# Optimization experiments

Measured on AMD Instinct MI355X. Metric: run time of the kernel, lower is better.

## Reference

```python
import jax, jax.numpy as jnp
import numpy as np

# Config mirrors CrossAttentionAudio2T(dim=768, n_head=12, num_frames=16, spec_frames=8,
# attn_all_frame=True, audio_patch=196, time_encoding=False, use_stpos=True)
B, T, N, NA, ST, D, H = 4, 8, 196, 196, 8, 768, 12
HD = D // H
SCALE = HD ** -0.5


def setup_inputs() -> dict:
    key = jax.random.key(0)
    ks = jax.random.split(key, 12)
    r = lambda k, s: jax.random.normal(k, s, dtype=jnp.float32)
    return dict(
        t_x=r(ks[0], (B, T * N, D)),
        audio=r(ks[1], (NA + 2, B * ST, D)),
        vmae_space_pos=SCALE * r(ks[2], (N, D)),
        audio_space_pos=SCALE * r(ks[3], (NA, D)),
        vmae_temporal_pos=SCALE * r(ks[4], (T, D)),
        audio_temporal_pos=SCALE * r(ks[5], (ST, D)),
        q_w=0.02 * r(ks[6], (D, D)),
        q_b=jnp.zeros((D,), jnp.float32),
        kv_w=0.02 * r(ks[7], (2 * D, D)),
        kv_b=jnp.zeros((2 * D,), jnp.float32),
        proj_w=0.02 * r(ks[8], (D, D)),
        proj_b=jnp.zeros((D,), jnp.float32),
    )


def reference(t_x, audio, vmae_space_pos, audio_space_pos, vmae_temporal_pos,
              audio_temporal_pos, q_w, q_b, kv_w, kv_b, proj_w, proj_b):
    # --- video query tokens: add spatial + temporal pos embeds ---
    x = t_x.reshape(B, T, N, D) + vmae_space_pos          # [B,T,N,D] + [N,D]
    x = x.transpose(0, 2, 1, 3) + vmae_temporal_pos       # [B,N,T,D] + [T,D]
    x = x.transpose(0, 2, 1, 3).reshape(B, T * N, D)      # 'b n t d -> b (t n) d'

    # --- audio key/value tokens: drop 2 lead tokens, add pos embeds ---
    a = audio[2:].reshape(NA, B, ST, D).transpose(1, 2, 0, 3)  # 'n (b t) d -> b t n d'
    a = a + audio_space_pos                                    # [B,ST,NA,D] + [NA,D]
    a = a.transpose(0, 2, 1, 3) + audio_temporal_pos           # [B,NA,ST,D] + [ST,D]
    a = a.reshape(B, NA * ST, D)                               # 'b n t d -> b (n t) d'

    # --- projections ---
    q = (x @ q_w.T + q_b).reshape(B, T * N, H, HD).transpose(0, 2, 1, 3)   # [B,H,Lq,HD]
    kv = (a @ kv_w.T + kv_b).reshape(B, NA * ST, 2, H, HD)
    k = kv[:, :, 0].transpose(0, 2, 1, 3)                                  # [B,H,Lk,HD]
    v = kv[:, :, 1].transpose(0, 2, 1, 3)

    # --- scaled dot-product cross-attention (full score matrix, as in source) ---
    attn = jax.nn.softmax(jnp.einsum('bhqd,bhkd->bhqk', q * SCALE, k), axis=-1)
    o = jnp.einsum('bhqk,bhkd->bhqd', attn, v)
    o = o.transpose(0, 2, 1, 3).reshape(B, T * N, D)
    return o @ proj_w.T + proj_b
```

## Files before the change

### kernel.cpp

```cpp
#include <hip/hip_runtime.h>

typedef short s8v __attribute__((ext_vector_type(8)));
typedef short s4v __attribute__((ext_vector_type(4)));
typedef float f4v __attribute__((ext_vector_type(4)));

#define LQ 1568
#define LK 1568
#define NH 12

__device__ __forceinline__ unsigned short f2bf(float f) {
  union { float f; unsigned u; } x; x.f = f;
  unsigned r = x.u + 0x7FFFu + ((x.u >> 16) & 1u);
  return (unsigned short)(r >> 16);
}


__global__ void prep_x(const float* __restrict__ t_x, const float* __restrict__ sp,
                       const float* __restrict__ tp, unsigned short* __restrict__ xb,
                       int total4) {
  int i = blockIdx.x * 256 + threadIdx.x;
  if (i >= total4) return;
  int d4 = (i % 192) * 4;
  int row = i / 192;
  int l = row % LQ;
  int t = l / 196, n = l % 196;
  float4 a  = *(const float4*)(t_x + (size_t)i * 4);
  float4 s  = *(const float4*)(sp + n * 768 + d4);
  float4 tt = *(const float4*)(tp + t * 768 + d4);
  ushort4 o;
  o.x = f2bf(a.x + s.x + tt.x);
  o.y = f2bf(a.y + s.y + tt.y);
  o.z = f2bf(a.z + s.z + tt.z);
  o.w = f2bf(a.w + s.w + tt.w);
  *(ushort4*)(xb + (size_t)i * 4) = o;
}

__global__ void prep_a(const float* __restrict__ audio, const float* __restrict__ asp,
                       const float* __restrict__ atp, unsigned short* __restrict__ ab,
                       int total4) {
  int i = blockIdx.x * 256 + threadIdx.x;
  if (i >= total4) return;
  int d4 = (i % 192) * 4;
  int row = i / 192;
  int b = row / LK;
  int r2 = row % LK;
  int na = r2 >> 3, ta = r2 & 7;
  const float* src = audio + ((size_t)(2 + na) * 32 + b * 8 + ta) * 768 + d4;
  float4 a  = *(const float4*)src;
  float4 s  = *(const float4*)(asp + na * 768 + d4);
  float4 tt = *(const float4*)(atp + ta * 768 + d4);
  ushort4 o;
  o.x = f2bf(a.x + s.x + tt.x);
  o.y = f2bf(a.y + s.y + tt.y);
  o.z = f2bf(a.z + s.z + tt.z);
  o.w = f2bf(a.w + s.w + tt.w);
  *(ushort4*)(ab + (size_t)i * 4) = o;
}

__global__ void conv_bf16(const float* __restrict__ src, unsigned short* __restrict__ dst,
                          int n4) {
  int i = blockIdx.x * 256 + threadIdx.x;
  if (i >= n4) return;
  float4 v = *(const float4*)(src + (size_t)i * 4);
  ushort4 o;
  o.x = f2bf(v.x); o.y = f2bf(v.y); o.z = f2bf(v.z); o.w = f2bf(v.w);
  *(ushort4*)(dst + (size_t)i * 4) = o;
}

__global__ __launch_bounds__(256, 2) void gemm_bt(
    const unsigned short* __restrict__ A, const unsigned short* __restrict__ W,
    const float* __restrict__ bias,
    unsigned short* __restrict__ out_a, unsigned short* __restrict__ out_b,
    float* __restrict__ out_f, int K, int N, int mode) {
  __shared__ __align__(16) unsigned short As[128 * 72];
  __shared__ __align__(16) unsigned short Bs[128 * 72];
  const int tid = threadIdx.x;
  const int lane = tid & 63, wave = tid >> 6;
  const int wm = wave & 1, wn = wave >> 1;
  const int l15 = lane & 15, quad = lane >> 4;
  const int row0 = blockIdx.x * 128;
  const int col0 = blockIdx.y * 128;

  f4v acc[4][4] = {};

  for (int k0 = 0; k0 < K; k0 += 64) {
    __syncthreads();
    for (int c = tid; c < 1024; c += 256) {
      int r = c >> 3, kc = c & 7;
      *(uint4*)(As + r * 72 + kc * 8) =
          *(const uint4*)(A + (size_t)(row0 + r) * K + k0 + kc * 8);
      *(uint4*)(Bs + r * 72 + kc * 8) =
          *(const uint4*)(W + (size_t)(col0 + r) * K + k0 + kc * 8);
    }
    __syncthreads();
#pragma unroll
    for (int kk = 0; kk < 2; ++kk) {
      s8v af[4], bf[4];
#pragma unroll
      for (int i = 0; i < 4; ++i) {
        af[i] = *(const s8v*)(As + (wm * 64 + i * 16 + l15) * 72 + kk * 32 + quad * 8);
        bf[i] = *(const s8v*)(Bs + (wn * 64 + i * 16 + l15) * 72 + kk * 32 + quad * 8);
      }
#pragma unroll
      for (int mi = 0; mi < 4; ++mi)
#pragma unroll
        for (int ni = 0; ni < 4; ++ni)
          acc[mi][ni] = __builtin_amdgcn_mfma_f32_16x16x32_bf16(af[mi], bf[ni],
                                                               acc[mi][ni], 0, 0, 0);
    }
  }

#pragma unroll
  for (int mi = 0; mi < 4; ++mi) {
    int rowg = row0 + wm * 64 + mi * 16 + quad * 4;
#pragma unroll
    for (int ni = 0; ni < 4; ++ni) {
      int colg = col0 + wn * 64 + ni * 16 + l15;
      float bv = bias[colg];
      if (mode == 1 && colg >= 768) {
        int oo = colg - 768;
        int h = oo >> 6, hd = oo & 63;
        int b = rowg / LK, l0 = rowg - b * LK;
        ushort4 pk;
        pk.x = f2bf(acc[mi][ni][0] + bv);
        pk.y = f2bf(acc[mi][ni][1] + bv);
        pk.z = f2bf(acc[mi][ni][2] + bv);
        pk.w = f2bf(acc[mi][ni][3] + bv);
        *(ushort4*)(out_b + ((((size_t)b * NH + h) * 392 + (l0 >> 2)) * 64 + hd) * 4) = pk;
        continue;
      }
#pragma unroll
      for (int r = 0; r < 4; ++r) {
        float v = acc[mi][ni][r] + bv;
        int row = rowg + r;
        if (mode == 0) {
          v *= 0.18033688011112042f;
          int b = row / LQ, l = row - b * LQ;
          int h = colg >> 6, hd = colg & 63;
          out_a[(((size_t)b * NH + h) * LQ + l) * 64 + hd] = f2bf(v);
        } else if (mode == 1) {
          int b = row / LK, l = row - b * LK;
          int h = colg >> 6, hd = colg & 63;
          out_a[(((size_t)b * NH + h) * LK + l) * 64 + hd] = f2bf(v);
        } else {
          out_f[(size_t)row * N + colg] = v;
        }
      }
    }
  }
}

__global__ __launch_bounds__(256, 3) void attn(
    const unsigned short* __restrict__ Q, const unsigned short* __restrict__ Kg,
    const unsigned short* __restrict__ Vsw, unsigned short* __restrict__ O) {
  __shared__ __align__(16) unsigned short Kl[112 * 72];
  __shared__ __align__(16) unsigned short Vl[112 * 64];
  const int tid = threadIdx.x;
  const int lane = tid & 63, wave = tid >> 6;
  const int l15 = lane & 15, quad = lane >> 4;
  const int bh = blockIdx.y;
  const int q0 = blockIdx.x * 128;
  const size_t base = (size_t)bh * LK * 64;

  s8v qf[2][2];
#pragma unroll
  for (int mt = 0; mt < 2; ++mt)
#pragma unroll
    for (int kk = 0; kk < 2; ++kk) {
      int row = q0 + wave * 32 + mt * 16 + l15;
      if (row > LQ - 1) row = LQ - 1;
      qf[mt][kk] = *(const s8v*)(Q + base + (size_t)row * 64 + kk * 32 + quad * 8);
    }

  f4v of[2][4] = {};
  float lr[2] = {0.0f, 0.0f};

  for (int k0 = 0; k0 < LK; k0 += 112) {
    __syncthreads();
    for (int c = tid; c < 896; c += 256) {
      int r = c >> 3, kc = c & 7;
      *(uint4*)(Kl + r * 72 + kc * 8) =
          *(const uint4*)(Kg + base + (size_t)(k0 + r) * 64 + kc * 8);
    }
    {
      const uint4* src = (const uint4*)(Vsw + base + (size_t)k0 * 64);
      uint4* dst = (uint4*)Vl;
      for (int c = tid; c < 896; c += 256) dst[c] = src[c];
    }
    __syncthreads();

#pragma unroll
    for (int nt = 0; nt < 7; ++nt) {
      s8v kf0 = *(const s8v*)(Kl + (nt * 16 + l15) * 72 + quad * 8);
      s8v kf1 = *(const s8v*)(Kl + (nt * 16 + l15) * 72 + 32 + quad * 8);
      s4v pf[2];
#pragma unroll
      for (int mt = 0; mt < 2; ++mt) {
        f4v s = {};
        s = __builtin_amdgcn_mfma_f32_16x16x32_bf16(kf0, qf[mt][0], s, 0, 0, 0);
        s = __builtin_amdgcn_mfma_f32_16x16x32_bf16(kf1, qf[mt][1], s, 0, 0, 0);
        float p0 = __builtin_amdgcn_exp2f(s[0]);
        float p1 = __builtin_amdgcn_exp2f(s[1]);
        float p2 = __builtin_amdgcn_exp2f(s[2]);
        float p3 = __builtin_amdgcn_exp2f(s[3]);
        lr[mt] += (p0 + p1) + (p2 + p3);
        union { float f; unsigned u; } a0, a1, a2, a3;
        a0.f = p0; a1.f = p1; a2.f = p2; a3.f = p3;
        union { uint2 u; s4v s; } pk;
        pk.u.x = __builtin_amdgcn_perm(a1.u, a0.u, 0x07060302u);
        pk.u.y = __builtin_amdgcn_perm(a3.u, a2.u, 0x07060302u);
        pf[mt] = pk.s;
      }
#pragma unroll
      for (int nd = 0; nd < 4; ++nd) {
        s4v vf = *(const s4v*)(Vl + ((nt * 4 + quad) << 8) + ((nd * 16 + l15) << 2));
        of[0][nd] = __builtin_amdgcn_mfma_f32_16x16x16bf16_1k(pf[0], vf, of[0][nd], 0, 0, 0);
        of[1][nd] = __builtin_amdgcn_mfma_f32_16x16x16bf16_1k(pf[1], vf, of[1][nd], 0, 0, 0);
      }
    }
  }

#pragma unroll
  for (int mt = 0; mt < 2; ++mt) {
    lr[mt] += __shfl_xor(lr[mt], 16);
    lr[mt] += __shfl_xor(lr[mt], 32);
  }

  const int b = bh / NH, h = bh - b * NH;
#pragma unroll
  for (int mt = 0; mt < 2; ++mt)
#pragma unroll
    for (int r = 0; r < 4; ++r) {
      int row = q0 + wave * 32 + mt * 16 + quad * 4 + r;
      if (row >= LQ) continue;
      float inv = 1.0f / __shfl(lr[mt], quad * 4 + r);
#pragma unroll
      for (int nd = 0; nd < 4; ++nd) {
        float v = of[mt][nd][r] * inv;
        O[((size_t)(b * LQ) + row) * 768 + h * 64 + nd * 16 + l15] = f2bf(v);
      }
    }
}

extern "C" void kernel_launch(void* const* d_in, const int* in_sizes, int n_in,
                              void* d_out, int out_size, void* d_ws, size_t ws_size,
                              hipStream_t stream) {
  const float* t_x    = (const float*)d_in[0];
  const float* audio  = (const float*)d_in[1];
  const float* sp     = (const float*)d_in[2];
  const float* asp    = (const float*)d_in[3];
  const float* tp     = (const float*)d_in[4];
  const float* atp    = (const float*)d_in[5];
  const float* q_w    = (const float*)d_in[6];
  const float* q_b    = (const float*)d_in[7];
  const float* kv_w   = (const float*)d_in[8];
  const float* kv_b   = (const float*)d_in[9];
  const float* proj_w = (const float*)d_in[10];
  const float* proj_b = (const float*)d_in[11];
  float* out = (float*)d_out;

  char* ws = (char*)d_ws;
  size_t off = 0;
  auto alloc = [&](size_t bytes) -> void* {
    void* p = ws + off;
    off += (bytes + 255) & ~(size_t)255;
    return p;
  };
  const size_t TOK = 6272;
  unsigned short* xb  = (unsigned short*)alloc(TOK * 768 * 2);
  unsigned short* ab  = (unsigned short*)alloc(TOK * 768 * 2);
  unsigned short* wq  = (unsigned short*)alloc(768 * 768 * 2);
  unsigned short* wkv = (unsigned short*)alloc(1536 * 768 * 2);
  unsigned short* wp  = (unsigned short*)alloc(768 * 768 * 2);
  unsigned short* Qs  = (unsigned short*)alloc(TOK * 768 * 2);
  unsigned short* Kb  = (unsigned short*)alloc(TOK * 768 * 2);
  unsigned short* Vb  = (unsigned short*)alloc(TOK * 768 * 2);

  dim3 blk(256);
  conv_bf16<<<dim3((768 * 768 / 4 + 255) / 256), blk, 0, stream>>>(q_w, wq, 768 * 768 / 4);
  conv_bf16<<<dim3((1536 * 768 / 4 + 255) / 256), blk, 0, stream>>>(kv_w, wkv, 1536 * 768 / 4);
  conv_bf16<<<dim3((768 * 768 / 4 + 255) / 256), blk, 0, stream>>>(proj_w, wp, 768 * 768 / 4);

  int total4 = (int)(TOK * 192);
  prep_x<<<dim3((total4 + 255) / 256), blk, 0, stream>>>(t_x, sp, tp, xb, total4);
  prep_a<<<dim3((total4 + 255) / 256), blk, 0, stream>>>(audio, asp, atp, ab, total4);

  gemm_bt<<<dim3(49, 6), blk, 0, stream>>>(xb, wq, q_b, Qs, nullptr, nullptr, 768, 768, 0);
  gemm_bt<<<dim3(49, 12), blk, 0, stream>>>(ab, wkv, kv_b, Kb, Vb, nullptr, 768, 1536, 1);

  attn<<<dim3(13, 48), blk, 0, stream>>>(Qs, Kb, Vb, xb );

  gemm_bt<<<dim3(49, 6), blk, 0, stream>>>(xb, wp, proj_b, nullptr, nullptr, out, 768, 768, 2);
}
```

Baseline: 285.9 us.

## Merge prep/convert/QKV launches and load GEMM tiles via global_load_lds

Combines the three weight conversions, the two input prep kernels, and the Q and KV projection GEMMs into single launches. This cuts launch overhead and lets the Q and KV work share one larger grid. The GEMM mainloop now copies tiles directly from global memory into LDS with global_load_lds and uses an unpadded 64-wide LDS stride. The risk is LDS bank conflicts on the fragment reads, since the padding is gone.

Result: faster. 245.4 us (-14.2%).

```diff
diff --git a/kernel.cpp b/kernel.cpp
--- a/kernel.cpp
+++ b/kernel.cpp
@@ -14,101 +14,126 @@
   return (unsigned short)(r >> 16);
 }
 
-
-__global__ void prep_x(const float* __restrict__ t_x, const float* __restrict__ sp,
-                       const float* __restrict__ tp, unsigned short* __restrict__ xb,
-                       int total4) {
+__global__ void prep_xa(const float* __restrict__ t_x, const float* __restrict__ audio,
+                        const float* __restrict__ sp, const float* __restrict__ asp,
+                        const float* __restrict__ tp, const float* __restrict__ atp,
+                        unsigned short* __restrict__ xb, unsigned short* __restrict__ ab,
+                        int total4) {
   int i = blockIdx.x * 256 + threadIdx.x;
-  if (i >= total4) return;
-  int d4 = (i % 192) * 4;
-  int row = i / 192;
-  int l = row % LQ;
-  int t = l / 196, n = l % 196;
-  float4 a  = *(const float4*)(t_x + (size_t)i * 4);
-  float4 s  = *(const float4*)(sp + n * 768 + d4);
-  float4 tt = *(const float4*)(tp + t * 768 + d4);
-  ushort4 o;
-  o.x = f2bf(a.x + s.x + tt.x);
-  o.y = f2bf(a.y + s.y + tt.y);
-  o.z = f2bf(a.z + s.z + tt.z);
-  o.w = f2bf(a.w + s.w + tt.w);
-  *(ushort4*)(xb + (size_t)i * 4) = o;
-}
-
-__global__ void prep_a(const float* __restrict__ audio, const float* __restrict__ asp,
-                       const float* __restrict__ atp, unsigned short* __restrict__ ab,
-                       int total4) {
+  if (i >= 2 * total4) return;
+  if (i < total4) {
+    int d4 = (i % 192) * 4;
+    int row = i / 192;
+    int l = row % LQ;
+    int t = l / 196, n = l % 196;
+    float4 a  = *(const float4*)(t_x + (size_t)i * 4);
+    float4 s  = *(const float4*)(sp + n * 768 + d4);
+    float4 tt = *(const float4*)(tp + t * 768 + d4);
+    ushort4 o;
+    o.x = f2bf(a.x + s.x + tt.x);
+    o.y = f2bf(a.y + s.y + tt.y);
+    o.z = f2bf(a.z + s.z + tt.z);
+    o.w = f2bf(a.w + s.w + tt.w);
+    *(ushort4*)(xb + (size_t)i * 4) = o;
+  } else {
+    i -= total4;
+    int d4 = (i % 192) * 4;
+    int row = i / 192;
+    int b = row / LK;
+    int r2 = row % LK;
+    int na = r2 >> 3, ta = r2 & 7;
+    const float* src = audio + ((size_t)(2 + na) * 32 + b * 8 + ta) * 768 + d4;
+    float4 a  = *(const float4*)src;
+    float4 s  = *(const float4*)(asp + na * 768 + d4);
+    float4 tt = *(const float4*)(atp + ta * 768 + d4);
+    ushort4 o;
+    o.x = f2bf(a.x + s.x + tt.x);
+    o.y = f2bf(a.y + s.y + tt.y);
+    o.z = f2bf(a.z + s.z + tt.z);
+    o.w = f2bf(a.w + s.w + tt.w);
+    *(ushort4*)(ab + (size_t)i * 4) = o;
+  }
+}
+
+__global__ void conv_w(const float* __restrict__ q_w, const float* __restrict__ kv_w,
+                       const float* __restrict__ proj_w, unsigned short* __restrict__ wq,
+                       unsigned short* __restrict__ wkv, unsigned short* __restrict__ wp) {
+  const int n1 = 768 * 768 / 4, n2 = 1536 * 768 / 4;
   int i = blockIdx.x * 256 + threadIdx.x;
-  if (i >= total4) return;
-  int d4 = (i % 192) * 4;
-  int row = i / 192;
-  int b = row / LK;
-  int r2 = row % LK;
-  int na = r2 >> 3, ta = r2 & 7;
-  const float* src = audio + ((size_t)(2 + na) * 32 + b * 8 + ta) * 768 + d4;
-  float4 a  = *(const float4*)src;
-  float4 s  = *(const float4*)(asp + na * 768 + d4);
-  float4 tt = *(const float4*)(atp + ta * 768 + d4);
-  ushort4 o;
-  o.x = f2bf(a.x + s.x + tt.x);
-  o.y = f2bf(a.y + s.y + tt.y);
-  o.z = f2bf(a.z + s.z + tt.z);
-  o.w = f2bf(a.w + s.w + tt.w);
-  *(ushort4*)(ab + (size_t)i * 4) = o;
-}
-
-__global__ void conv_bf16(const float* __restrict__ src, unsigned short* __restrict__ dst,
-                          int n4) {
-  int i = blockIdx.x * 256 + threadIdx.x;
-  if (i >= n4) return;
-  float4 v = *(const float4*)(src + (size_t)i * 4);
+  const float* src; unsigned short* dst; int j = i;
+  if (i < n1)               { src = q_w;    dst = wq;  }
+  else if (i < n1 + n2)     { src = kv_w;   dst = wkv; j = i - n1; }
+  else if (i < 2 * n1 + n2) { src = proj_w; dst = wp;  j = i - n1 - n2; }
+  else return;
+  float4 v = *(const float4*)(src + (size_t)j * 4);
   ushort4 o;
   o.x = f2bf(v.x); o.y = f2bf(v.y); o.z = f2bf(v.z); o.w = f2bf(v.w);
-  *(ushort4*)(dst + (size_t)i * 4) = o;
-}
-
-__global__ __launch_bounds__(256, 2) void gemm_bt(
+  *(ushort4*)(dst + (size_t)j * 4) = o;
+}
+
+__device__ __forceinline__ void gemm_mainloop(
     const unsigned short* __restrict__ A, const unsigned short* __restrict__ W,
-    const float* __restrict__ bias,
-    unsigned short* __restrict__ out_a, unsigned short* __restrict__ out_b,
-    float* __restrict__ out_f, int K, int N, int mode) {
-  __shared__ __align__(16) unsigned short As[128 * 72];
-  __shared__ __align__(16) unsigned short Bs[128 * 72];
+    int K, int row0, int col0,
+    unsigned short* As, unsigned short* Bs, f4v acc[4][4]) {
+  const int tid = threadIdx.x;
+  const int lane = tid & 63, wave = tid >> 6;
+  const int wm = wave & 1, wn = wave >> 1;
+  const int l15 = lane & 15, quad = lane >> 4;
+  const int lr = tid >> 3, lc = (tid & 7) * 8;
+
+  for (int k0 = 0; k0 < K; k0 += 64) {
+    __syncthreads();
+#pragma unroll
+    for (int it = 0; it < 4; ++it) {
+      int row = lr + it * 32;
+      __builtin_amdgcn_global_load_lds(
+          (const __attribute__((address_space(1))) unsigned int*)(A + (size_t)(row0 + row) * K + k0 + lc),
+          (__attribute__((address_space(3))) unsigned int*)(As + row * 64 + lc), 16, 0, 0);
+      __builtin_amdgcn_global_load_lds(
+          (const __attribute__((address_space(1))) unsigned int*)(W + (size_t)(col0 + row) * K + k0 + lc),
+          (__attribute__((address_space(3))) unsigned int*)(Bs + row * 64 + lc), 16, 0, 0);
+    }
+    __syncthreads();
+#pragma unroll
+    for (int kk = 0; kk < 2; ++kk) {
+      s8v af[4], bf[4];
+#pragma unroll
+      for (int i = 0; i < 4; ++i) {
+        af[i] = *(const s8v*)(As + (wm * 64 + i * 16 + l15) * 64 + kk * 32 + quad * 8);
+        bf[i] = *(const s8v*)(Bs + (wn * 64 + i * 16 + l15) * 64 + kk * 32 + quad * 8);
+      }
+#pragma unroll
+      for (int mi = 0; mi < 4; ++mi)
+#pragma unroll
+        for (int ni = 0; ni < 4; ++ni)
+          acc[mi][ni] = __builtin_amdgcn_mfma_f32_16x16x32_bf16(af[mi], bf[ni],
+                                                               acc[mi][ni], 0, 0, 0);
+    }
+  }
+}
+
+__global__ __launch_bounds__(256, 2) void gemm_qkv(
+    const unsigned short* __restrict__ xb, const unsigned short* __restrict__ ab,
+    const unsigned short* __restrict__ wq, const unsigned short* __restrict__ wkv,
+    const float* __restrict__ q_b, const float* __restrict__ kv_b,
+    unsigned short* __restrict__ Qs, unsigned short* __restrict__ Kb,
+    unsigned short* __restrict__ Vb) {
+  __shared__ __align__(16) unsigned short As[128 * 64];
+  __shared__ __align__(16) unsigned short Bs[128 * 64];
   const int tid = threadIdx.x;
   const int lane = tid & 63, wave = tid >> 6;
   const int wm = wave & 1, wn = wave >> 1;
   const int l15 = lane & 15, quad = lane >> 4;
   const int row0 = blockIdx.x * 128;
-  const int col0 = blockIdx.y * 128;
+  const int y = blockIdx.y;
+  const bool isQ = (y < 6);
+  const int col0 = (isQ ? y : y - 6) * 128;
+  const unsigned short* A = isQ ? xb : ab;
+  const unsigned short* W = isQ ? wq : wkv;
+  const float* bias = isQ ? q_b : kv_b;
 
   f4v acc[4][4] = {};
-
-  for (int k0 = 0; k0 < K; k0 += 64) {
-    __syncthreads();
-    for (int c = tid; c < 1024; c += 256) {
-      int r = c >> 3, kc = c & 7;
-      *(uint4*)(As + r * 72 + kc * 8) =
-          *(const uint4*)(A + (size_t)(row0 + r) * K + k0 + kc * 8);
-      *(uint4*)(Bs + r * 72 + kc * 8) =
-          *(const uint4*)(W + (size_t)(col0 + r) * K + k0 + kc * 8);
-    }
-    __syncthreads();
-#pragma unroll
-    for (int kk = 0; kk < 2; ++kk) {
-      s8v af[4], bf[4];
-#pragma unroll
-      for (int i = 0; i < 4; ++i) {
-        af[i] = *(const s8v*)(As + (wm * 64 + i * 16 + l15) * 72 + kk * 32 + quad * 8);
-        bf[i] = *(const s8v*)(Bs + (wn * 64 + i * 16 + l15) * 72 + kk * 32 + quad * 8);
-      }
-#pragma unroll
-      for (int mi = 0; mi < 4; ++mi)
-#pragma unroll
-        for (int ni = 0; ni < 4; ++ni)
-          acc[mi][ni] = __builtin_amdgcn_mfma_f32_16x16x32_bf16(af[mi], bf[ni],
-                                                               acc[mi][ni], 0, 0, 0);
-    }
-  }
+  gemm_mainloop(A, W, 768, row0, col0, As, Bs, acc);
 
 #pragma unroll
   for (int mi = 0; mi < 4; ++mi) {
@@ -117,7 +142,7 @@
     for (int ni = 0; ni < 4; ++ni) {
       int colg = col0 + wn * 64 + ni * 16 + l15;
       float bv = bias[colg];
-      if (mode == 1 && colg >= 768) {
+      if (!isQ && colg >= 768) {
         int oo = colg - 768;
         int h = oo >> 6, hd = oo & 63;
         int b = rowg / LK, l0 = rowg - b * LK;
@@ -126,26 +151,51 @@
         pk.y = f2bf(acc[mi][ni][1] + bv);
         pk.z = f2bf(acc[mi][ni][2] + bv);
         pk.w = f2bf(acc[mi][ni][3] + bv);
-        *(ushort4*)(out_b + ((((size_t)b * NH + h) * 392 + (l0 >> 2)) * 64 + hd) * 4) = pk;
+        *(ushort4*)(Vb + ((((size_t)b * NH + h) * 392 + (l0 >> 2)) * 64 + hd) * 4) = pk;
         continue;
       }
 #pragma unroll
       for (int r = 0; r < 4; ++r) {
         float v = acc[mi][ni][r] + bv;
         int row = rowg + r;
-        if (mode == 0) {
+        int b = row / LQ, l = row - b * LQ;
+        int h = colg >> 6, hd = colg & 63;
+        if (isQ) {
           v *= 0.18033688011112042f;
-          int b = row / LQ, l = row - b * LQ;
-          int h = colg >> 6, hd = colg & 63;
-          out_a[(((size_t)b * NH + h) * LQ + l) * 64 + hd] = f2bf(v);
-        } else if (mode == 1) {
-          int b = row / LK, l = row - b * LK;
-          int h = colg >> 6, hd = colg & 63;
-          out_a[(((size_t)b * NH + h) * LK + l) * 64 + hd] = f2bf(v);
+          Qs[(((size_t)b * NH + h) * LQ + l) * 64 + hd] = f2bf(v);
         } else {
-          out_f[(size_t)row * N + colg] = v;
+          Kb[(((size_t)b * NH + h) * LK + l) * 64 + hd] = f2bf(v);
         }
       }
+    }
+  }
+}
+
+__global__ __launch_bounds__(256, 2) void gemm_proj(
+    const unsigned short* __restrict__ A, const unsigned short* __restrict__ W,
+    const float* __restrict__ bias, float* __restrict__ out) {
+  __shared__ __align__(16) unsigned short As[128 * 64];
+  __shared__ __align__(16) unsigned short Bs[128 * 64];
+  const int tid = threadIdx.x;
+  const int lane = tid & 63, wave = tid >> 6;
+  const int wm = wave & 1, wn = wave >> 1;
+  const int l15 = lane & 15, quad = lane >> 4;
+  const int row0 = blockIdx.x * 128;
+  const int col0 = blockIdx.y * 128;
+
+  f4v acc[4][4] = {};
+  gemm_mainloop(A, W, 768, row0, col0, As, Bs, acc);
+
+#pragma unroll
+  for (int mi = 0; mi < 4; ++mi) {
+    int rowg = row0 + wm * 64 + mi * 16 + quad * 4;
+#pragma unroll
+    for (int ni = 0; ni < 4; ++ni) {
+      int colg = col0 + wn * 64 + ni * 16 + l15;
+      float bv = bias[colg];
+#pragma unroll
+      for (int r = 0; r < 4; ++r)
+        out[(size_t)(rowg + r) * 768 + colg] = acc[mi][ni][r] + bv;
     }
   }
 }
@@ -277,18 +327,16 @@
   unsigned short* Vb  = (unsigned short*)alloc(TOK * 768 * 2);
 
   dim3 blk(256);
-  conv_bf16<<<dim3((768 * 768 / 4 + 255) / 256), blk, 0, stream>>>(q_w, wq, 768 * 768 / 4);
-  conv_bf16<<<dim3((1536 * 768 / 4 + 255) / 256), blk, 0, stream>>>(kv_w, wkv, 1536 * 768 / 4);
-  conv_bf16<<<dim3((768 * 768 / 4 + 255) / 256), blk, 0, stream>>>(proj_w, wp, 768 * 768 / 4);
+  const int n1 = 768 * 768 / 4, n2 = 1536 * 768 / 4;
+  conv_w<<<dim3((2 * n1 + n2 + 255) / 256), blk, 0, stream>>>(q_w, kv_w, proj_w, wq, wkv, wp);
 
   int total4 = (int)(TOK * 192);
-  prep_x<<<dim3((total4 + 255) / 256), blk, 0, stream>>>(t_x, sp, tp, xb, total4);
-  prep_a<<<dim3((total4 + 255) / 256), blk, 0, stream>>>(audio, asp, atp, ab, total4);
-
-  gemm_bt<<<dim3(49, 6), blk, 0, stream>>>(xb, wq, q_b, Qs, nullptr, nullptr, 768, 768, 0);
-  gemm_bt<<<dim3(49, 12), blk, 0, stream>>>(ab, wkv, kv_b, Kb, Vb, nullptr, 768, 1536, 1);
+  prep_xa<<<dim3((2 * total4 + 255) / 256), blk, 0, stream>>>(t_x, audio, sp, asp, tp, atp,
+                                                              xb, ab, total4);
+
+  gemm_qkv<<<dim3(49, 18), blk, 0, stream>>>(xb, ab, wq, wkv, q_b, kv_b, Qs, Kb, Vb);
 
   attn<<<dim3(13, 48), blk, 0, stream>>>(Qs, Kb, Vb, xb );
 
-  gemm_bt<<<dim3(49, 6), blk, 0, stream>>>(xb, wp, proj_b, nullptr, nullptr, out, 768, 768, 2);
-}
+  gemm_proj<<<dim3(49, 6), blk, 0, stream>>>(xb, wp, proj_b, out);
+}
```
